# Optimization experiments

Hardware: AMD Instinct MI355X
Metric: run time of the kernel (lower is better)

## Reference

```python
import jax, jax.numpy as jnp
import numpy as np

B, S, T = 512, 512, 128


def setup_inputs() -> dict:
    key = jax.random.key(0)
    k1, k2, k3, k4, k5 = jax.random.split(key, 5)
    emissions = jax.random.normal(k1, (B, S, T), dtype=jnp.float32)
    tags = jax.random.randint(k2, (B, S), 0, T, dtype=jnp.int32)
    mask = jnp.ones((B, S), dtype=jnp.int32)
    start_transitions = jax.random.uniform(k3, (T,), minval=-0.1, maxval=0.1, dtype=jnp.float32)
    end_transitions = jax.random.uniform(k4, (T,), minval=-0.1, maxval=0.1, dtype=jnp.float32)
    transitions = jax.random.uniform(k5, (T, T), minval=-0.1, maxval=0.1, dtype=jnp.float32)
    return {"emissions": emissions, "tags": tags, "mask": mask,
            "start_transitions": start_transitions,
            "end_transitions": end_transitions,
            "transitions": transitions}


def reference(emissions, tags, mask, start_transitions, end_transitions, transitions):
    b, s, t = emissions.shape
    maskf = mask.astype(emissions.dtype)
    barange = jnp.arange(b)

    # ---- numerator: score of the gold path (vectorized over timesteps) ----
    score = start_transitions[tags[:, 0]] + emissions[barange, 0, tags[:, 0]]
    # transition scores tags[i-1] -> tags[i], shape (B, S-1)
    trans_steps = transitions[tags[:, :-1], tags[:, 1:]]
    # emission score of gold tag at each step, shape (B, S)
    em_steps = jnp.take_along_axis(emissions, tags[:, :, None], axis=2)[:, :, 0]
    score = score + jnp.sum((trans_steps + em_steps[:, 1:]) * maskf[:, 1:], axis=1)
    seq_ends = mask.astype(jnp.int32).sum(axis=1) - 1
    last_tags = tags[barange, seq_ends]
    score = score + end_transitions[last_tags]

    # ---- denominator: log partition via forward recurrence (lax.scan) ----
    init = start_transitions[None, :] + emissions[:, 0, :]  # (B, T)

    def step(scores, inp):
        em_i, m_i = inp  # (B, T), (B,)
        # (B, T_prev, T_next) semiring matmul in log-space
        nxt = jax.nn.logsumexp(
            scores[:, :, None] + transitions[None, :, :] + em_i[:, None, :], axis=1)
        scores = jnp.where(m_i[:, None] > 0, nxt, scores)
        return scores, None

    ems = jnp.moveaxis(emissions[:, 1:, :], 1, 0)  # (S-1, B, T)
    ms = jnp.moveaxis(mask[:, 1:], 1, 0)           # (S-1, B)
    final, _ = jax.lax.scan(step, init, (ems, ms))
    denom = jax.nn.logsumexp(final + end_transitions[None, :], axis=1)  # (B,)

    return jnp.sum(score - denom)
```

## Files before the change

kernel.cpp:

```cpp
#include <hip/hip_runtime.h>
#include <math.h>


#define T 128
#define SLEN 512
#define BATCH 512

typedef float v2f __attribute__((ext_vector_type(2)));

static __device__ __forceinline__ float dpp_xor1(float x) {
    return __int_as_float(__builtin_amdgcn_update_dpp(
        0, __float_as_int(x), 0xB1, 0xF, 0xF, true));
}
static __device__ __forceinline__ float dpp_xor2(float x) {
    return __int_as_float(__builtin_amdgcn_update_dpp(
        0, __float_as_int(x), 0x4E, 0xF, 0xF, true));
}
static __device__ __forceinline__ float swz_xor4(float x) {
    return __int_as_float(__builtin_amdgcn_ds_swizzle(__float_as_int(x), 0x101F));
}
static __device__ __forceinline__ void lgkm_barrier() {
    asm volatile("s_waitcnt lgkmcnt(0)\n\ts_barrier" ::: "memory");
}
static __device__ __forceinline__ int pslot(int j) {
    return j ^ (((j >> 5) & 3) << 2);
}

__global__ __launch_bounds__(256, 2) void fwd_kernel(
    const float* __restrict__ em, const int* __restrict__ tags,
    const int* __restrict__ mask, const float* __restrict__ startT,
    const float* __restrict__ endT, const float* __restrict__ trans,
    float* __restrict__ ws)
{
    const int tid  = threadIdx.x;
    const int lane = tid & 63;
    const int w    = tid >> 6;
    const int rg   = lane & 7;
    const int cw   = lane >> 3;
    const int g    = 8 * w + cw;
    const int b    = blockIdx.x;
    const int rb0  = rg & 1, rb1 = (rg >> 1) & 1, rb2 = (rg >> 2) & 1;
    const int mycol = 4 * g + 2 * rb0 + rb1;

    const float* emb = em + (size_t)b * SLEN * T;
    const int*   mk  = mask + (size_t)b * SLEN;

    __shared__ __align__(16) float p_lds[2][T];
    __shared__ float reds[4], redn[4];
    __shared__ int   redc[4];

    int rbase[4], rslot[4];
#pragma unroll
    for (int k = 0; k < 4; ++k) {
        rbase[k] = 16 * rg + 4 * ((k + rg) & 3);
        rslot[k] = pslot(rbase[k]);
    }
    const int wslot = pslot(mycol);

    v2f Elo[4][4], Ehi[4][4];
    {
        const int cb = 4 * g;
#pragma unroll
        for (int k = 0; k < 4; ++k) {
            const float* t0p = trans + (rbase[k] + 0) * T + cb;
            const float* t1p = t0p + T;
            const float* t2p = t1p + T;
            const float* t3p = t2p + T;
#pragma unroll
            for (int c = 0; c < 4; ++c) {
                Elo[k][c] = (v2f){ __expf(t0p[c]), __expf(t1p[c]) };
                Ehi[k][c] = (v2f){ __expf(t2p[c]), __expf(t3p[c]) };
            }
        }
    }

    float pprev = __expf(startT[mycol] + emb[mycol]);
    p_lds[1][wslot] = pprev;
    double Ld = 0.0;

    float emv[4], emn[4];
    int   mkv[4], mkn[4];
#pragma unroll
    for (int k = 0; k < 4; ++k) {
        emv[k] = __expf(emb[(1 + k) * T + mycol]);
        mkv[k] = mk[1 + k];
    }
    lgkm_barrier();

    for (int s0 = 1; s0 < SLEN; s0 += 4) {
#pragma unroll
        for (int k = 0; k < 4; ++k) {
            int ss = s0 + 4 + k; ss = (ss < SLEN) ? ss : (SLEN - 1);
            emn[k] = emb[ss * T + mycol];
            mkn[k] = mk[ss];
        }
#pragma unroll
        for (int k = 0; k < 4; ++k) {
            const int s = s0 + k;
            if (s < SLEN) {
                const int cur = (1 + k) & 1;
                const float sref0 = p_lds[cur][0];
                const float srefc = fmaxf(sref0, 1e-30f);
                const float cc = __builtin_amdgcn_rcpf(srefc);
                Ld += (double)__logf(srefc);

                v2f pk0[4], pk1[4];
#pragma unroll
                for (int kk = 0; kk < 4; ++kk) {
                    const float4 pv = *(const float4*)&p_lds[cur][rslot[kk]];
                    pk0[kk] = (v2f){ pv.x, pv.y };
                    pk1[kk] = (v2f){ pv.z, pv.w };
                }
                v2f acc[4];
#pragma unroll
                for (int c = 0; c < 4; ++c)
                    acc[c] = pk0[0] * Elo[0][c];
#pragma unroll
                for (int c = 0; c < 4; ++c)
                    acc[c] = __builtin_elementwise_fma(pk1[0], Ehi[0][c], acc[c]);
#pragma unroll
                for (int kk = 1; kk < 4; ++kk) {
#pragma unroll
                    for (int c = 0; c < 4; ++c) {
                        acc[c] = __builtin_elementwise_fma(pk0[kk], Elo[kk][c], acc[c]);
                        acc[c] = __builtin_elementwise_fma(pk1[kk], Ehi[kk][c], acc[c]);
                    }
                }
                float sv[4];
#pragma unroll
                for (int c = 0; c < 4; ++c) sv[c] = acc[c].x + acc[c].y;

                float v1[2];
#pragma unroll
                for (int c = 0; c < 2; ++c)
                    v1[c] = (rb0 ? sv[c + 2] : sv[c])
                          + dpp_xor1(rb0 ? sv[c] : sv[c + 2]);
                const float v2_ = (rb1 ? v1[1] : v1[0])
                                + dpp_xor2(rb1 ? v1[0] : v1[1]);
                const float t = v2_ + swz_xor4(v2_);

                const float pn = t * (emv[k] * cc);
                const float pm = pprev * cc;
                pprev = (mkv[k] > 0) ? pn : pm;
                p_lds[cur ^ 1][wslot] = pprev;
                lgkm_barrier();
            }
        }
#pragma unroll
        for (int k = 0; k < 4; ++k) { emv[k] = __expf(emn[k]); mkv[k] = mkn[k]; }
    }

    const float eendv = __expf(endT[mycol]);
    float sm = pprev * eendv;
#pragma unroll
    for (int off = 32; off; off >>= 1) sm += __shfl_xor(sm, off);
    if (lane == 0) reds[w] = sm;

    const int* tg = tags + (size_t)b * SLEN;
    float nv = 0.f; int cnt = 0;
#pragma unroll
    for (int rep = 0; rep < 2; ++rep) {
        const int s = tid + 256 * rep;
        const int mm = mk[s];
        cnt += (mm != 0);
        if (s >= 1 && mm > 0)
            nv += trans[tg[s - 1] * T + tg[s]] + emb[s * T + tg[s]];
    }
#pragma unroll
    for (int off = 32; off; off >>= 1) {
        nv  += __shfl_xor(nv, off);
        cnt += __shfl_xor(cnt, off);
    }
    if (lane == 0) { redn[w] = nv; redc[w] = cnt; }
    __syncthreads();
    if (tid == 0) {
        float ssum = 0.f, nsum = 0.f; int seqlen = 0;
#pragma unroll
        for (int i = 0; i < 4; ++i) {
            ssum += reds[i]; nsum += redn[i]; seqlen += redc[i];
        }
        const float denom = __logf(0.5f * ssum) + (float)Ld;
        const int t0g = tg[0], tl = tg[seqlen - 1];
        ws[b] = (startT[t0g] + emb[t0g] + endT[tl] + nsum) - denom;
    }
}

__global__ __launch_bounds__(256) void reduce_kernel(
    const float* __restrict__ ws, float* __restrict__ out)
{
    const int t = threadIdx.x;
    float local = 0.f;
    for (int i = t; i < BATCH; i += 256) local += ws[i];
    __shared__ float rf[256];
    rf[t] = local;
    __syncthreads();
    for (int off = 128; off > 0; off >>= 1) {
        if (t < off) rf[t] += rf[t + off];
        __syncthreads();
    }
    if (t == 0) out[0] = rf[0];
}

extern "C" void kernel_launch(void* const* d_in, const int* in_sizes, int n_in,
                              void* d_out, int out_size, void* d_ws, size_t ws_size,
                              hipStream_t stream)
{
    const float* emissions = (const float*)d_in[0];
    const int*   tags      = (const int*)d_in[1];
    const int*   mask      = (const int*)d_in[2];
    const float* startT    = (const float*)d_in[3];
    const float* endT      = (const float*)d_in[4];
    const float* trans     = (const float*)d_in[5];
    float* out = (float*)d_out;
    float* ws  = (float*)d_ws;

    fwd_kernel<<<BATCH, 256, 0, stream>>>(emissions, tags, mask, startT, endT, trans, ws);
    reduce_kernel<<<1, 256, 0, stream>>>(ws, out);
}
```

Measured before the change: 369.3 us.

## Process two batch sequences per block to share transition registers and barriers

Each block now runs the forward recurrence for two batch elements at once, interleaving their FMA chains and sharing the exp(transitions) registers and the per-step barrier. The grid is halved to 256 blocks. This is meant to amortise barrier and LDS latency across two independent chains and give more ILP per step. In exchange it raises register pressure and halves the block count. With 256 CUs on MI355X that leaves roughly one block per CU, so occupancy and latency hiding drop.

```diff
diff --git a/kernel.cpp b/kernel.cpp
--- a/kernel.cpp
+++ b/kernel.cpp
@@ -38,16 +38,19 @@
     const int rg   = lane & 7;
     const int cw   = lane >> 3;
     const int g    = 8 * w + cw;
-    const int b    = blockIdx.x;
+    const int bA   = 2 * blockIdx.x;
+    const int bB   = bA + 1;
     const int rb0  = rg & 1, rb1 = (rg >> 1) & 1, rb2 = (rg >> 2) & 1;
     const int mycol = 4 * g + 2 * rb0 + rb1;
 
-    const float* emb = em + (size_t)b * SLEN * T;
-    const int*   mk  = mask + (size_t)b * SLEN;
-
-    __shared__ __align__(16) float p_lds[2][T];
-    __shared__ float reds[4], redn[4];
-    __shared__ int   redc[4];
+    const float* embA = em + (size_t)bA * SLEN * T;
+    const float* embB = em + (size_t)bB * SLEN * T;
+    const int*   mkA  = mask + (size_t)bA * SLEN;
+    const int*   mkB  = mask + (size_t)bB * SLEN;
+
+    __shared__ __align__(16) float p_lds[2][2][T];
+    __shared__ float reds[2][4], redn[2][4];
+    __shared__ int   redc[2][4];
 
     int rbase[4], rslot[4];
 #pragma unroll
@@ -74,16 +77,20 @@
         }
     }
 
-    float pprev = __expf(startT[mycol] + emb[mycol]);
-    p_lds[1][wslot] = pprev;
-    double Ld = 0.0;
-
-    float emv[4], emn[4];
-    int   mkv[4], mkn[4];
+    float ppA = __expf(startT[mycol] + embA[mycol]);
+    float ppB = __expf(startT[mycol] + embB[mycol]);
+    p_lds[0][1][wslot] = ppA;
+    p_lds[1][1][wslot] = ppB;
+    double LdA = 0.0, LdB = 0.0;
+
+    float emvA[4], emnA[4], emvB[4], emnB[4];
+    int   mkvA[4], mknA[4], mkvB[4], mknB[4];
 #pragma unroll
     for (int k = 0; k < 4; ++k) {
-        emv[k] = __expf(emb[(1 + k) * T + mycol]);
-        mkv[k] = mk[1 + k];
+        emvA[k] = __expf(embA[(1 + k) * T + mycol]);
+        emvB[k] = __expf(embB[(1 + k) * T + mycol]);
+        mkvA[k] = mkA[1 + k];
+        mkvB[k] = mkB[1 + k];
     }
     lgkm_barrier();
 
@@ -91,97 +98,135 @@
 #pragma unroll
         for (int k = 0; k < 4; ++k) {
             int ss = s0 + 4 + k; ss = (ss < SLEN) ? ss : (SLEN - 1);
-            emn[k] = emb[ss * T + mycol];
-            mkn[k] = mk[ss];
+            emnA[k] = embA[ss * T + mycol];
+            emnB[k] = embB[ss * T + mycol];
+            mknA[k] = mkA[ss];
+            mknB[k] = mkB[ss];
         }
 #pragma unroll
         for (int k = 0; k < 4; ++k) {
             const int s = s0 + k;
             if (s < SLEN) {
                 const int cur = (1 + k) & 1;
-                const float sref0 = p_lds[cur][0];
-                const float srefc = fmaxf(sref0, 1e-30f);
-                const float cc = __builtin_amdgcn_rcpf(srefc);
-                Ld += (double)__logf(srefc);
-
-                v2f pk0[4], pk1[4];
+                const float srefA = fmaxf(p_lds[0][cur][0], 1e-30f);
+                const float srefB = fmaxf(p_lds[1][cur][0], 1e-30f);
+                const float ccA = __builtin_amdgcn_rcpf(srefA);
+                const float ccB = __builtin_amdgcn_rcpf(srefB);
+                LdA += (double)__logf(srefA);
+                LdB += (double)__logf(srefB);
+
+                v2f pkA0[4], pkA1[4], pkB0[4], pkB1[4];
 #pragma unroll
                 for (int kk = 0; kk < 4; ++kk) {
-                    const float4 pv = *(const float4*)&p_lds[cur][rslot[kk]];
-                    pk0[kk] = (v2f){ pv.x, pv.y };
-                    pk1[kk] = (v2f){ pv.z, pv.w };
-                }
-                v2f acc[4];
-#pragma unroll
-                for (int c = 0; c < 4; ++c)
-                    acc[c] = pk0[0] * Elo[0][c];
-#pragma unroll
-                for (int c = 0; c < 4; ++c)
-                    acc[c] = __builtin_elementwise_fma(pk1[0], Ehi[0][c], acc[c]);
+                    const float4 pa = *(const float4*)&p_lds[0][cur][rslot[kk]];
+                    const float4 pb = *(const float4*)&p_lds[1][cur][rslot[kk]];
+                    pkA0[kk] = (v2f){ pa.x, pa.y }; pkA1[kk] = (v2f){ pa.z, pa.w };
+                    pkB0[kk] = (v2f){ pb.x, pb.y }; pkB1[kk] = (v2f){ pb.z, pb.w };
+                }
+                v2f accA[4], accB[4];
+#pragma unroll
+                for (int c = 0; c < 4; ++c) {
+                    accA[c] = pkA0[0] * Elo[0][c];
+                    accB[c] = pkB0[0] * Elo[0][c];
+                }
+#pragma unroll
+                for (int c = 0; c < 4; ++c) {
+                    accA[c] = __builtin_elementwise_fma(pkA1[0], Ehi[0][c], accA[c]);
+                    accB[c] = __builtin_elementwise_fma(pkB1[0], Ehi[0][c], accB[c]);
+                }
 #pragma unroll
                 for (int kk = 1; kk < 4; ++kk) {
 #pragma unroll
                     for (int c = 0; c < 4; ++c) {
-                        acc[c] = __builtin_elementwise_fma(pk0[kk], Elo[kk][c], acc[c]);
-                        acc[c] = __builtin_elementwise_fma(pk1[kk], Ehi[kk][c], acc[c]);
+                        accA[c] = __builtin_elementwise_fma(pkA0[kk], Elo[kk][c], accA[c]);
+                        accB[c] = __builtin_elementwise_fma(pkB0[kk], Elo[kk][c], accB[c]);
+                        accA[c] = __builtin_elementwise_fma(pkA1[kk], Ehi[kk][c], accA[c]);
+                        accB[c] = __builtin_elementwise_fma(pkB1[kk], Ehi[kk][c], accB[c]);
                     }
                 }
-                float sv[4];
-#pragma unroll
-                for (int c = 0; c < 4; ++c) sv[c] = acc[c].x + acc[c].y;
-
-                float v1[2];
-#pragma unroll
-                for (int c = 0; c < 2; ++c)
-                    v1[c] = (rb0 ? sv[c + 2] : sv[c])
-                          + dpp_xor1(rb0 ? sv[c] : sv[c + 2]);
-                const float v2_ = (rb1 ? v1[1] : v1[0])
-                                + dpp_xor2(rb1 ? v1[0] : v1[1]);
-                const float t = v2_ + swz_xor4(v2_);
-
-                const float pn = t * (emv[k] * cc);
-                const float pm = pprev * cc;
-                pprev = (mkv[k] > 0) ? pn : pm;
-                p_lds[cur ^ 1][wslot] = pprev;
+                float svA[4], svB[4];
+#pragma unroll
+                for (int c = 0; c < 4; ++c) {
+                    svA[c] = accA[c].x + accA[c].y;
+                    svB[c] = accB[c].x + accB[c].y;
+                }
+
+                float v1A[2], v1B[2];
+#pragma unroll
+                for (int c = 0; c < 2; ++c) {
+                    v1A[c] = (rb0 ? svA[c + 2] : svA[c])
+                           + dpp_xor1(rb0 ? svA[c] : svA[c + 2]);
+                    v1B[c] = (rb0 ? svB[c + 2] : svB[c])
+                           + dpp_xor1(rb0 ? svB[c] : svB[c + 2]);
+                }
+                const float v2A = (rb1 ? v1A[1] : v1A[0])
+                                + dpp_xor2(rb1 ? v1A[0] : v1A[1]);
+                const float v2B = (rb1 ? v1B[1] : v1B[0])
+                                + dpp_xor2(rb1 ? v1B[0] : v1B[1]);
+                const float tA = v2A + swz_xor4(v2A);
+                const float tB = v2B + swz_xor4(v2B);
+
+                const float pnA = tA * (emvA[k] * ccA);
+                const float pnB = tB * (emvB[k] * ccB);
+                ppA = (mkvA[k] > 0) ? pnA : (ppA * ccA);
+                ppB = (mkvB[k] > 0) ? pnB : (ppB * ccB);
+                p_lds[0][cur ^ 1][wslot] = ppA;
+                p_lds[1][cur ^ 1][wslot] = ppB;
                 lgkm_barrier();
             }
         }
 #pragma unroll
-        for (int k = 0; k < 4; ++k) { emv[k] = __expf(emn[k]); mkv[k] = mkn[k]; }
+        for (int k = 0; k < 4; ++k) {
+            emvA[k] = __expf(emnA[k]); mkvA[k] = mknA[k];
+            emvB[k] = __expf(emnB[k]); mkvB[k] = mknB[k];
+        }
     }
 
     const float eendv = __expf(endT[mycol]);
-    float sm = pprev * eendv;
-#pragma unroll
-    for (int off = 32; off; off >>= 1) sm += __shfl_xor(sm, off);
-    if (lane == 0) reds[w] = sm;
-
-    const int* tg = tags + (size_t)b * SLEN;
-    float nv = 0.f; int cnt = 0;
+    float smA = ppA * eendv, smB = ppB * eendv;
+#pragma unroll
+    for (int off = 32; off; off >>= 1) {
+        smA += __shfl_xor(smA, off);
+        smB += __shfl_xor(smB, off);
+    }
+    if (lane == 0) { reds[0][w] = smA; reds[1][w] = smB; }
+
+    const int* tgA = tags + (size_t)bA * SLEN;
+    const int* tgB = tags + (size_t)bB * SLEN;
+    float nvA = 0.f, nvB = 0.f; int cntA = 0, cntB = 0;
 #pragma unroll
     for (int rep = 0; rep < 2; ++rep) {
         const int s = tid + 256 * rep;
-        const int mm = mk[s];
-        cnt += (mm != 0);
-        if (s >= 1 && mm > 0)
-            nv += trans[tg[s - 1] * T + tg[s]] + emb[s * T + tg[s]];
+        const int mmA = mkA[s], mmB = mkB[s];
+        cntA += (mmA != 0);
+        cntB += (mmB != 0);
+        if (s >= 1 && mmA > 0)
+            nvA += trans[tgA[s - 1] * T + tgA[s]] + embA[s * T + tgA[s]];
+        if (s >= 1 && mmB > 0)
+            nvB += trans[tgB[s - 1] * T + tgB[s]] + embB[s * T + tgB[s]];
     }
 #pragma unroll
     for (int off = 32; off; off >>= 1) {
-        nv  += __shfl_xor(nv, off);
-        cnt += __shfl_xor(cnt, off);
-    }
-    if (lane == 0) { redn[w] = nv; redc[w] = cnt; }
+        nvA += __shfl_xor(nvA, off); cntA += __shfl_xor(cntA, off);
+        nvB += __shfl_xor(nvB, off); cntB += __shfl_xor(cntB, off);
+    }
+    if (lane == 0) { redn[0][w] = nvA; redc[0][w] = cntA;
+                     redn[1][w] = nvB; redc[1][w] = cntB; }
     __syncthreads();
     if (tid == 0) {
-        float ssum = 0.f, nsum = 0.f; int seqlen = 0;
+        float ssA = 0.f, nsA = 0.f, ssB = 0.f, nsB = 0.f;
+        int slA = 0, slB = 0;
 #pragma unroll
         for (int i = 0; i < 4; ++i) {
-            ssum += reds[i]; nsum += redn[i]; seqlen += redc[i];
-        }
-        const float denom = __logf(0.5f * ssum) + (float)Ld;
-        const int t0g = tg[0], tl = tg[seqlen - 1];
-        ws[b] = (startT[t0g] + emb[t0g] + endT[tl] + nsum) - denom;
+            ssA += reds[0][i]; nsA += redn[0][i]; slA += redc[0][i];
+            ssB += reds[1][i]; nsB += redn[1][i]; slB += redc[1][i];
+        }
+        const float denomA = __logf(0.5f * ssA) + (float)LdA;
+        const float denomB = __logf(0.5f * ssB) + (float)LdB;
+        const int tA0 = tgA[0], tAl = tgA[slA - 1];
+        const int tB0 = tgB[0], tBl = tgB[slB - 1];
+        ws[bA] = (startT[tA0] + embA[tA0] + endT[tAl] + nsA) - denomA;
+        ws[bB] = (startT[tB0] + embB[tB0] + endT[tBl] + nsB) - denomB;
     }
 }
 
@@ -214,6 +259,6 @@
     float* out = (float*)d_out;
     float* ws  = (float*)d_ws;
 
-    fwd_kernel<<<BATCH, 256, 0, stream>>>(emissions, tags, mask, startT, endT, trans, ws);
+    fwd_kernel<<<BATCH / 2, 256, 0, stream>>>(emissions, tags, mask, startT, endT, trans, ws);
     reduce_kernel<<<1, 256, 0, stream>>>(ws, out);
 }
```

Result: slower. 453.6 us (+22.8%).

## Use 512 threads per batch row with one column per 4-lane group

Applied to the files above, without the earlier changes.

The forward-recurrence block doubles from 256 to 512 threads. Each 4-lane group now owns one output tag column and each lane covers 32 previous-tag rows, where before each lane computed partial sums for 4 columns over 16 rows. The per-step cross-lane reduction shrinks to two DPP xor steps and drops the ds_swizzle, the register-held transition exponentials fall from 32 to 16 v2f, and FMA work per lane is halved. In exchange every step's barrier now spans 8 waves instead of 4, and each column's value is computed redundantly by 4 lanes, so the final sum over the block is scaled by 0.25.

```diff
diff --git a/kernel.cpp b/kernel.cpp
--- a/kernel.cpp
+++ b/kernel.cpp
@@ -16,9 +16,6 @@
     return __int_as_float(__builtin_amdgcn_update_dpp(
         0, __float_as_int(x), 0x4E, 0xF, 0xF, true));
 }
-static __device__ __forceinline__ float swz_xor4(float x) {
-    return __int_as_float(__builtin_amdgcn_ds_swizzle(__float_as_int(x), 0x101F));
-}
 static __device__ __forceinline__ void lgkm_barrier() {
     asm volatile("s_waitcnt lgkmcnt(0)\n\ts_barrier" ::: "memory");
 }
@@ -26,7 +23,7 @@
     return j ^ (((j >> 5) & 3) << 2);
 }
 
-__global__ __launch_bounds__(256, 2) void fwd_kernel(
+__global__ __launch_bounds__(512, 4) void fwd_kernel(
     const float* __restrict__ em, const int* __restrict__ tags,
     const int* __restrict__ mask, const float* __restrict__ startT,
     const float* __restrict__ endT, const float* __restrict__ trans,
@@ -35,47 +32,34 @@
     const int tid  = threadIdx.x;
     const int lane = tid & 63;
     const int w    = tid >> 6;
-    const int rg   = lane & 7;
-    const int cw   = lane >> 3;
-    const int g    = 8 * w + cw;
+    const int rg   = lane & 3;
+    const int cg   = lane >> 2;
     const int b    = blockIdx.x;
-    const int rb0  = rg & 1, rb1 = (rg >> 1) & 1, rb2 = (rg >> 2) & 1;
-    const int mycol = 4 * g + 2 * rb0 + rb1;
+    const int mycol = 16 * w + cg;
 
     const float* emb = em + (size_t)b * SLEN * T;
     const int*   mk  = mask + (size_t)b * SLEN;
 
     __shared__ __align__(16) float p_lds[2][T];
-    __shared__ float reds[4], redn[4];
-    __shared__ int   redc[4];
+    __shared__ float reds[8], redn[8];
+    __shared__ int   redc[8];
 
-    int rbase[4], rslot[4];
+    int rslot[8];
 #pragma unroll
-    for (int k = 0; k < 4; ++k) {
-        rbase[k] = 16 * rg + 4 * ((k + rg) & 3);
-        rslot[k] = pslot(rbase[k]);
-    }
+    for (int k = 0; k < 8; ++k)
+        rslot[k] = (32 * rg + 4 * k) ^ (rg << 2);
     const int wslot = pslot(mycol);
 
-    v2f Elo[4][4], Ehi[4][4];
-    {
-        const int cb = 4 * g;
+    v2f Elo[8], Ehi[8];
 #pragma unroll
-        for (int k = 0; k < 4; ++k) {
-            const float* t0p = trans + (rbase[k] + 0) * T + cb;
-            const float* t1p = t0p + T;
-            const float* t2p = t1p + T;
-            const float* t3p = t2p + T;
-#pragma unroll
-            for (int c = 0; c < 4; ++c) {
-                Elo[k][c] = (v2f){ __expf(t0p[c]), __expf(t1p[c]) };
-                Ehi[k][c] = (v2f){ __expf(t2p[c]), __expf(t3p[c]) };
-            }
-        }
+    for (int k = 0; k < 8; ++k) {
+        const float* tp = trans + (32 * rg + 4 * k) * T + mycol;
+        Elo[k] = (v2f){ __expf(tp[0 * T]), __expf(tp[1 * T]) };
+        Ehi[k] = (v2f){ __expf(tp[2 * T]), __expf(tp[3 * T]) };
     }
 
     float pprev = __expf(startT[mycol] + emb[mycol]);
-    p_lds[1][wslot] = pprev;
+    if (rg == 0) p_lds[1][wslot] = pprev;
     double Ld = 0.0;
 
     float emv[4], emn[4];
@@ -99,50 +83,34 @@
             const int s = s0 + k;
             if (s < SLEN) {
                 const int cur = (1 + k) & 1;
-                const float sref0 = p_lds[cur][0];
-                const float srefc = fmaxf(sref0, 1e-30f);
+                const float srefc = fmaxf(p_lds[cur][0], 1e-30f);
                 const float cc = __builtin_amdgcn_rcpf(srefc);
                 Ld += (double)__logf(srefc);
 
-                v2f pk0[4], pk1[4];
+                v2f pk0[8], pk1[8];
 #pragma unroll
-                for (int kk = 0; kk < 4; ++kk) {
-                    const float4 pv = *(const float4*)&p_lds[cur][rslot[kk]];
-                    pk0[kk] = (v2f){ pv.x, pv.y };
-                    pk1[kk] = (v2f){ pv.z, pv.w };
+                for (int k2 = 0; k2 < 8; ++k2) {
+                    const float4 pv = *(const float4*)&p_lds[cur][rslot[k2]];
+                    pk0[k2] = (v2f){ pv.x, pv.y };
+                    pk1[k2] = (v2f){ pv.z, pv.w };
                 }
-                v2f acc[4];
+                v2f accE = pk0[0] * Elo[0];
+                v2f accO = pk1[0] * Ehi[0];
 #pragma unroll
-                for (int c = 0; c < 4; ++c)
-                    acc[c] = pk0[0] * Elo[0][c];
-#pragma unroll
-                for (int c = 0; c < 4; ++c)
-                    acc[c] = __builtin_elementwise_fma(pk1[0], Ehi[0][c], acc[c]);
-#pragma unroll
-                for (int kk = 1; kk < 4; ++kk) {
-#pragma unroll
-                    for (int c = 0; c < 4; ++c) {
-                        acc[c] = __builtin_elementwise_fma(pk0[kk], Elo[kk][c], acc[c]);
-                        acc[c] = __builtin_elementwise_fma(pk1[kk], Ehi[kk][c], acc[c]);
-                    }
+                for (int k2 = 1; k2 < 8; ++k2) {
+                    accE = __builtin_elementwise_fma(pk0[k2], Elo[k2], accE);
+                    accO = __builtin_elementwise_fma(pk1[k2], Ehi[k2], accO);
                 }
-                float sv[4];
-#pragma unroll
-                for (int c = 0; c < 4; ++c) sv[c] = acc[c].x + acc[c].y;
+                const v2f accT = accE + accO;
+                const float sv = accT.x + accT.y;
 
-                float v1[2];
-#pragma unroll
-                for (int c = 0; c < 2; ++c)
-                    v1[c] = (rb0 ? sv[c + 2] : sv[c])
-                          + dpp_xor1(rb0 ? sv[c] : sv[c + 2]);
-                const float v2_ = (rb1 ? v1[1] : v1[0])
-                                + dpp_xor2(rb1 ? v1[0] : v1[1]);
-                const float t = v2_ + swz_xor4(v2_);
+                float t = sv + dpp_xor1(sv);
+                t = t + dpp_xor2(t);
 
                 const float pn = t * (emv[k] * cc);
                 const float pm = pprev * cc;
                 pprev = (mkv[k] > 0) ? pn : pm;
-                p_lds[cur ^ 1][wslot] = pprev;
+                if (rg == 0) p_lds[cur ^ 1][wslot] = pprev;
                 lgkm_barrier();
             }
         }
@@ -158,9 +126,8 @@
 
     const int* tg = tags + (size_t)b * SLEN;
     float nv = 0.f; int cnt = 0;
-#pragma unroll
-    for (int rep = 0; rep < 2; ++rep) {
-        const int s = tid + 256 * rep;
+    {
+        const int s = tid;
         const int mm = mk[s];
         cnt += (mm != 0);
         if (s >= 1 && mm > 0)
@@ -176,10 +143,10 @@
     if (tid == 0) {
         float ssum = 0.f, nsum = 0.f; int seqlen = 0;
 #pragma unroll
-        for (int i = 0; i < 4; ++i) {
+        for (int i = 0; i < 8; ++i) {
             ssum += reds[i]; nsum += redn[i]; seqlen += redc[i];
         }
-        const float denom = __logf(0.5f * ssum) + (float)Ld;
+        const float denom = __logf(0.25f * ssum) + (float)Ld;
         const int t0g = tg[0], tl = tg[seqlen - 1];
         ws[b] = (startT[t0g] + emb[t0g] + endT[tl] + nsum) - denom;
     }
@@ -214,6 +181,6 @@
     float* out = (float*)d_out;
     float* ws  = (float*)d_ws;
 
-    fwd_kernel<<<BATCH, 256, 0, stream>>>(emissions, tags, mask, startT, endT, trans, ws);
+    fwd_kernel<<<BATCH, 512, 0, stream>>>(emissions, tags, mask, startT, endT, trans, ws);
     reduce_kernel<<<1, 256, 0, stream>>>(ws, out);
 }
```

After: 392.2 us. 1.06x slower.
